# Performance work log

Measured on AMD Instinct MI355X. Metric: run time of the kernel, lower is better.

Reference implementation:

```python
import jax, jax.numpy as jnp
import numpy as np

B, T, C, H = 8, 2048, 1024, 64  # batch, seq_len, num_embed, size_head


def setup_inputs() -> dict:
    key = jax.random.key(0)
    kx, kq, kk, kv = jax.random.split(key, 4)
    return {
        "x": jax.random.normal(kx, (B, T, C), dtype=jnp.float32),
        "Wq": jax.random.normal(kq, (C, H), dtype=jnp.float32) * 0.02,
        "Wk": jax.random.normal(kk, (C, H), dtype=jnp.float32) * 0.02,
        "Wv": jax.random.normal(kv, (C, H), dtype=jnp.float32) * 0.02,
    }


def reference(x, Wq, Wk, Wv):
    # x: [B, T, C]; single-head causal self-attention.
    # NOTE: original scales by num_channels = x.shape[-1] (= C), not head dim.
    num_channels = x.shape[-1]
    q = jnp.einsum("btc,ch->bth", x, Wq)
    k = jnp.einsum("btc,ch->bth", x, Wk)
    v = jnp.einsum("btc,ch->bth", x, Wv)
    w = jnp.einsum("bqh,bkh->bqk", q, k) * (num_channels ** -0.5)  # [B,T,T]
    causal = jnp.tril(jnp.ones((x.shape[1], x.shape[1]), dtype=bool))
    w = jnp.where(causal, w, -jnp.inf)
    w = jax.nn.softmax(w, axis=-1)
    # dropout is identity in eval/reference mode
    out = jnp.einsum("bqk,bkh->bqh", w, v)  # [B,T,H]
    return out
```

## Files before the change

kernel.cpp:

```cpp
#include <hip/hip_runtime.h>
#include <hip/hip_bf16.h>
#include <stdint.h>

#define Bn 8
#define Tn 2048
#define Cn 1024
#define Hn 64

typedef __attribute__((ext_vector_type(8))) short bf16x8;
typedef __attribute__((ext_vector_type(4))) short bf16x4;
typedef __attribute__((ext_vector_type(4))) float f32x4;

#if defined(__HIP_DEVICE_COMPILE__) && !__has_builtin(__builtin_amdgcn_mfma_f32_16x16x16bf16_1k)
#error "mfma_f32_16x16x16bf16_1k required on gfx950"
#endif
#define MFMA16(a, b, c) __builtin_amdgcn_mfma_f32_16x16x16bf16_1k(a, b, c, 0, 0, 0)
#define MFMA32(a, b, c) __builtin_amdgcn_mfma_f32_16x16x32_bf16(a, b, c, 0, 0, 0)

__device__ __forceinline__ unsigned short f2bf(float f) {
  union { float f; unsigned int u; } v; v.f = f;
  unsigned int u = v.u;
  u = u + 0x7fffu + ((u >> 16) & 1u);
  return (unsigned short)(u >> 16);
}

__device__ __forceinline__ void gload16(const void* g, void* l) {
  __builtin_amdgcn_global_load_lds(
      (const __attribute__((address_space(1))) unsigned int*)g,
      (__attribute__((address_space(3))) unsigned int*)l, 16, 0, 0);
}

__global__ __launch_bounds__(256) void k_prep(const float* __restrict__ Wq,
                                              const float* __restrict__ Wk,
                                              const float* __restrict__ Wv,
                                              unsigned short* __restrict__ Wt) {
  const int m = blockIdx.x >> 6;
  const int h = blockIdx.x & 63;
  const float* W = (m == 0) ? Wq : (m == 1) ? Wk : Wv;
  const int tid = threadIdx.x;
  unsigned short* dst = Wt + ((size_t)(m * 64 + h)) * 1024;
#pragma unroll
  for (int j = 0; j < 4; ++j) {
    int c = j * 256 + tid;
    dst[c] = f2bf(W[(size_t)c * 64 + h]);
  }
}

__global__ __launch_bounds__(256, 1) void k_qkv(const float* __restrict__ x,
                                                const unsigned short* __restrict__ Wt,
                                                unsigned short* __restrict__ Q,
                                                unsigned short* __restrict__ K,
                                                unsigned short* __restrict__ Vt) {
  __shared__ __align__(16) char smem[81920];

  const int tid = threadIdx.x;
  const int lane = tid & 63;
  const int wid = __builtin_amdgcn_readfirstlane(tid >> 6);
  const int l15 = lane & 15, g = lane >> 4;
  const int r0 = blockIdx.x * 64;

  f32x4 acc[12];
#pragma unroll
  for (int j = 0; j < 12; ++j)
#pragma unroll
    for (int r = 0; r < 4; ++r) acc[j][r] = 0.f;

  auto stage = [&](int buf, int kt) {
    char* base = smem + buf * 40960;
    const int k0 = kt * 64;
#pragma unroll
    for (int j = 0; j < 4; ++j) {
      const int c = wid * 4 + j;
      const int row = c * 4 + (lane >> 4);
      const int lg = (lane & 15) ^ (row & 7);
      gload16(x + (size_t)(r0 + row) * 1024 + k0 + lg * 4,
              base + c * 1024);
    }
#pragma unroll
    for (int j = 0; j < 6; ++j) {
      const int c = j * 4 + wid;
      const int row = c * 8 + (lane >> 3);
      const int lg = (lane & 7) ^ (row & 7);
      gload16(Wt + (size_t)row * 1024 + k0 + lg * 8,
              base + 16384 + c * 1024);
    }
  };

  stage(0, 0);
  const int myrow = wid * 16 + l15;
  const int rs = myrow & 7;
  for (int kt = 0; kt < 16; ++kt) {
    const int cur = kt & 1;
    __syncthreads();
    if (kt < 15) stage(cur ^ 1, kt + 1);
    const char* base = smem + cur * 40960;
    const float* xf = (const float*)base;
    const unsigned short* wf = (const unsigned short*)(base + 16384);
#pragma unroll
    for (int kf = 0; kf < 2; ++kf) {
      f32x4 x0 = *(const f32x4*)&xf[myrow * 64 + (((kf * 8 + 2 * g) ^ rs) * 4)];
      f32x4 x1 = *(const f32x4*)&xf[myrow * 64 + (((kf * 8 + 2 * g + 1) ^ rs) * 4)];
      bf16x8 a;
      a[0] = (short)f2bf(x0[0]); a[1] = (short)f2bf(x0[1]);
      a[2] = (short)f2bf(x0[2]); a[3] = (short)f2bf(x0[3]);
      a[4] = (short)f2bf(x1[0]); a[5] = (short)f2bf(x1[1]);
      a[6] = (short)f2bf(x1[2]); a[7] = (short)f2bf(x1[3]);
#pragma unroll
      for (int nf = 0; nf < 12; ++nf) {
        const int row = nf * 16 + l15;
        bf16x8 b = *(const bf16x8*)&wf[row * 64 + (((kf * 4 + g) ^ (row & 7)) * 8)];
        acc[nf] = MFMA32(a, b, acc[nf]);
      }
    }
  }

  unsigned short (*os)[200] = (unsigned short (*)[200])smem;
#pragma unroll
  for (int nf = 0; nf < 12; ++nf)
#pragma unroll
    for (int r = 0; r < 4; ++r)
      os[wid * 16 + 4 * g + r][nf * 16 + l15] = f2bf(acc[nf][r]);
  __syncthreads();

  const int b = r0 >> 11;
  const int t0 = r0 & 2047;
#pragma unroll
  for (int j = 0; j < 2; ++j) {
    int u = j * 256 + tid;
    int row = u >> 3, ch = u & 7;
    *(uint4*)(Q + (size_t)(r0 + row) * 64 + ch * 8) = *(const uint4*)&os[row][ch * 8];
    *(uint4*)(K + (size_t)(r0 + row) * 64 + ch * 8) = *(const uint4*)&os[row][64 + ch * 8];
  }
#pragma unroll
  for (int j = 0; j < 2; ++j) {
    int u = j * 256 + tid;
    int h = u >> 3, tc = (u & 7) * 8;
    unsigned short tmp[8];
#pragma unroll
    for (int r = 0; r < 8; ++r) tmp[r] = os[tc + r][128 + h];
    *(uint4*)(Vt + ((size_t)b * 64 + h) * 2048 + t0 + tc) = *(const uint4*)tmp;
  }
}

__global__ __launch_bounds__(256, 3) void k_attn_coop(const unsigned short* __restrict__ Q,
                                                      const unsigned short* __restrict__ K,
                                                      const unsigned short* __restrict__ Vt,
                                                      float* __restrict__ out,
                                                      float* __restrict__ po,
                                                      float* __restrict__ pml) {
  __shared__ __align__(16) unsigned short lds[2][8192];

  const int tid = threadIdx.x;
  const int lane = tid & 63;
  const int l15 = lane & 15, g = lane >> 4;
  const int wid = __builtin_amdgcn_readfirstlane(tid >> 6);

  const int raw = blockIdx.x;
  const int bi = (raw & 7) * 144 + (raw >> 3);
  const int b = bi / 144;
  const int id = bi - b * 144;
  int gq = 0;
#pragma unroll
  for (int t = 1; t < 8; ++t)
    if (id >= 2 * t * (t + 1)) gq = t;
  const int rem = id - 2 * gq * (gq + 1);
  const int ql = rem / (gq + 1);
  const int s = rem - ql * (gq + 1);
  const int qt = 4 * gq + ql;
  const int qblk = qt * 64;
  const int klo = 256 * s;
  const int khi = min(klo + 256, qblk + 64);
  const int nt = (khi - klo + 63) >> 6;
  const int q0w = qblk + wid * 16;

  const unsigned short* Qb = Q + (size_t)b * Tn * Hn;
  const unsigned short* Kb = K + (size_t)b * Tn * Hn;
  const unsigned short* Vb = Vt + (size_t)b * Hn * Tn;

  bf16x8 bq0 = *(const bf16x8*)(Qb + (size_t)(q0w + l15) * 64 + g * 8);
  bf16x8 bq1 = *(const bf16x8*)(Qb + (size_t)(q0w + l15) * 64 + 32 + g * 8);

  f32x4 o[4];
#pragma unroll
  for (int hf = 0; hf < 4; ++hf)
#pragma unroll
    for (int r = 0; r < 4; ++r) o[hf][r] = 0.f;
  float m = -1e30f, lsum = 0.f;
  const float sc = 0.03125f * 1.44269504088896f;

  auto stage = [&](int buf, int k0) {
    unsigned short* tb = &lds[buf][0];
#pragma unroll
    for (int j = 0; j < 4; ++j) {
      const int p = wid * 256 + j * 64 + lane;
      const unsigned short* src;
      if (wid < 2) {
        const int row = p >> 3, c = p & 7;
        src = Kb + (size_t)(k0 + row) * 64 + ((c ^ (row & 7)) * 8);
      } else {
        const int q = p - 512;
        const int h = q >> 3, c = q & 7;
        src = Vb + (size_t)h * Tn + k0 + ((c ^ (h & 7)) * 8);
      }
      gload16(src, tb + wid * 2048 + j * 512);
    }
  };

  stage(0, klo);
  __syncthreads();

  for (int t = 0; t < nt; ++t) {
    const int cur = t & 1;
    const int k0 = klo + t * 64;
    if (t + 1 < nt) stage(cur ^ 1, klo + (t + 1) * 64);

    const unsigned short* kt = &lds[cur][0];
    const unsigned short* vt = &lds[cur][4096];

    f32x4 sacc[4];
#pragma unroll
    for (int kc = 0; kc < 4; ++kc) {
      const int row = kc * 16 + l15;
      const int sw = row & 7;
      bf16x8 ka = *(const bf16x8*)&kt[row * 64 + ((g ^ sw) * 8)];
      bf16x8 kb2 = *(const bf16x8*)&kt[row * 64 + (((4 + g) ^ sw) * 8)];
#pragma unroll
      for (int r = 0; r < 4; ++r) sacc[kc][r] = 0.f;
      sacc[kc] = MFMA32(ka, bq0, sacc[kc]);
      sacc[kc] = MFMA32(kb2, bq1, sacc[kc]);
    }
    float sv[4][4];
    if (k0 + 63 > q0w) {
      const int q = q0w + l15;
#pragma unroll
      for (int kc = 0; kc < 4; ++kc)
#pragma unroll
        for (int r = 0; r < 4; ++r) {
          int key = k0 + kc * 16 + 4 * g + r;
          sv[kc][r] = (key <= q) ? sacc[kc][r] * sc : -1e30f;
        }
    } else {
#pragma unroll
      for (int kc = 0; kc < 4; ++kc)
#pragma unroll
        for (int r = 0; r < 4; ++r) sv[kc][r] = sacc[kc][r] * sc;
    }
    float pm = sv[0][0];
#pragma unroll
    for (int kc = 0; kc < 4; ++kc)
#pragma unroll
      for (int r = 0; r < 4; ++r) pm = fmaxf(pm, sv[kc][r]);
    if (__any(pm > m + 8.f)) {
      pm = fmaxf(pm, __shfl_xor(pm, 16));
      pm = fmaxf(pm, __shfl_xor(pm, 32));
      float mn = fmaxf(m, pm);
      float alpha = exp2f(m - mn);
      lsum *= alpha;
      float an[4];
#pragma unroll
      for (int r = 0; r < 4; ++r) an[r] = __shfl(alpha, 4 * g + r);
#pragma unroll
      for (int hf = 0; hf < 4; ++hf)
#pragma unroll
        for (int r = 0; r < 4; ++r) o[hf][r] *= an[r];
      m = mn;
    }
    float ts = 0.f;
#pragma unroll
    for (int kc = 0; kc < 4; ++kc)
#pragma unroll
      for (int r = 0; r < 4; ++r) { sv[kc][r] = exp2f(sv[kc][r] - m); ts += sv[kc][r]; }
    ts += __shfl_xor(ts, 16);
    ts += __shfl_xor(ts, 32);
    lsum += ts;
    bf16x4 pa[4];
#pragma unroll
    for (int kc = 0; kc < 4; ++kc) {
      pa[kc][0] = (short)f2bf(sv[kc][0]); pa[kc][1] = (short)f2bf(sv[kc][1]);
      pa[kc][2] = (short)f2bf(sv[kc][2]); pa[kc][3] = (short)f2bf(sv[kc][3]);
    }
    bf16x4 vf[4][4];
#pragma unroll
    for (int hf = 0; hf < 4; ++hf) {
      const int h = hf * 16 + l15, hs = h & 7;
#pragma unroll
      for (int kc = 0; kc < 4; ++kc) {
        const int gran = (kc * 2 + (g >> 1)) ^ hs;
        vf[hf][kc] = *(const bf16x4*)&vt[h * 64 + gran * 8 + (g & 1) * 4];
      }
    }
#pragma unroll
    for (int hf = 0; hf < 4; ++hf)
#pragma unroll
      for (int kc = 0; kc < 4; ++kc)
        o[hf] = MFMA16(pa[kc], vf[hf][kc], o[hf]);

    __syncthreads();
  }

  if (qt >= 4) {
    const int slot = b * 140 + id - 4;
    float* pob = po + (size_t)slot * 4096;
#pragma unroll
    for (int hf = 0; hf < 4; ++hf)
#pragma unroll
      for (int r = 0; r < 4; ++r)
        pob[(16 * wid + 4 * g + r) * 64 + hf * 16 + l15] = o[hf][r];
    if (lane < 16) {
      pml[(size_t)slot * 128 + 16 * wid + l15] = m;
      pml[(size_t)slot * 128 + 64 + 16 * wid + l15] = lsum;
    }
  } else {
    const float il = 1.f / lsum;
    float iln[4];
#pragma unroll
    for (int r = 0; r < 4; ++r) iln[r] = __shfl(il, 4 * g + r);
    float* ob = out + ((size_t)b * Tn + q0w) * 64;
#pragma unroll
    for (int hf = 0; hf < 4; ++hf)
#pragma unroll
      for (int r = 0; r < 4; ++r)
        ob[(size_t)(4 * g + r) * 64 + hf * 16 + l15] = o[hf][r] * iln[r];
  }
}

__global__ __launch_bounds__(256) void k_comb(const float* __restrict__ po,
                                              const float* __restrict__ pml,
                                              float* __restrict__ out) {
  const int qt = 4 + blockIdx.x;
  const int b = blockIdx.y;
  const int gq = qt >> 2, ql = qt & 3;
  const int nseg = gq + 1;
  const int base = b * 140 + 2 * gq * (gq + 1) + ql * (gq + 1) - 4;
  const int r = threadIdx.x >> 2;
  const int cg = threadIdx.x & 3;

  float mv[8], lv[8], M = -1e30f;
#pragma unroll
  for (int s = 0; s < 8; ++s)
    if (s < nseg) {
      mv[s] = pml[(size_t)(base + s) * 128 + r];
      lv[s] = pml[(size_t)(base + s) * 128 + 64 + r];
      M = fmaxf(M, mv[s]);
    }
  float w[8], L = 0.f;
#pragma unroll
  for (int s = 0; s < 8; ++s)
    if (s < nseg) { w[s] = exp2f(mv[s] - M); L += w[s] * lv[s]; }

  float acc[16];
#pragma unroll
  for (int c = 0; c < 16; ++c) acc[c] = 0.f;
#pragma unroll
  for (int s = 0; s < 8; ++s)
    if (s < nseg) {
      const float* pb = po + (size_t)(base + s) * 4096 + r * 64 + cg * 16;
#pragma unroll
      for (int j = 0; j < 4; ++j) {
        float4 v = *(const float4*)(pb + 4 * j);
        acc[4 * j + 0] += w[s] * v.x; acc[4 * j + 1] += w[s] * v.y;
        acc[4 * j + 2] += w[s] * v.z; acc[4 * j + 3] += w[s] * v.w;
      }
    }
  const float invL = 1.f / L;
  float* ob = out + ((size_t)b * Tn + qt * 64 + r) * 64 + cg * 16;
#pragma unroll
  for (int j = 0; j < 4; ++j) {
    float4 v;
    v.x = acc[4 * j + 0] * invL; v.y = acc[4 * j + 1] * invL;
    v.z = acc[4 * j + 2] * invL; v.w = acc[4 * j + 3] * invL;
    *(float4*)(ob + 4 * j) = v;
  }
}

__global__ __launch_bounds__(256, 2) void k_attn_wave(const unsigned short* __restrict__ Q,
                                                      const unsigned short* __restrict__ K,
                                                      const unsigned short* __restrict__ Vt,
                                                      float* __restrict__ out) {
  const int tid = threadIdx.x;
  const int lane = tid & 63;
  const int l15 = lane & 15, g = lane >> 4;
  const int wid = tid >> 6;
  const int task = blockIdx.x * 4 + wid;
  const int b = task >> 7, qt = task & 127;
  const int q0 = qt * 16;
  const int nt = (q0 + 16 + 63) >> 6;

  const unsigned short* Qb = Q + (size_t)b * Tn * Hn;
  const unsigned short* Kb = K + (size_t)b * Tn * Hn;
  const unsigned short* Vb = Vt + (size_t)b * Hn * Tn;

  bf16x8 bq0 = *(const bf16x8*)(Qb + (size_t)(q0 + l15) * 64 + g * 8);
  bf16x8 bq1 = *(const bf16x8*)(Qb + (size_t)(q0 + l15) * 64 + 32 + g * 8);

  f32x4 o[4];
#pragma unroll
  for (int hf = 0; hf < 4; ++hf)
#pragma unroll
    for (int r = 0; r < 4; ++r) o[hf][r] = 0.f;
  float m = -1e30f, lsum = 0.f;
  const float sc = 0.03125f * 1.44269504088896f;

  for (int t = 0; t < nt; ++t) {
    const int k0 = t * 64;
    bf16x4 vf[4][4];
#pragma unroll
    for (int hf = 0; hf < 4; ++hf) {
      const unsigned short* vrow = Vb + (size_t)(hf * 16 + l15) * Tn + k0 + 4 * g;
#pragma unroll
      for (int kc = 0; kc < 4; ++kc) vf[hf][kc] = *(const bf16x4*)(vrow + kc * 16);
    }
    f32x4 sacc[4];
#pragma unroll
    for (int kc = 0; kc < 4; ++kc) {
      const unsigned short* kp = Kb + (size_t)(k0 + kc * 16 + l15) * 64 + g * 8;
      bf16x8 ka = *(const bf16x8*)kp;
      bf16x8 kb2 = *(const bf16x8*)(kp + 32);
#pragma unroll
      for (int r = 0; r < 4; ++r) sacc[kc][r] = 0.f;
      sacc[kc] = MFMA32(ka, bq0, sacc[kc]);
      sacc[kc] = MFMA32(kb2, bq1, sacc[kc]);
    }
    float sv[4][4];
    if (k0 + 63 > q0) {
      const int q = q0 + l15;
#pragma unroll
      for (int kc = 0; kc < 4; ++kc)
#pragma unroll
        for (int r = 0; r < 4; ++r) {
          int key = k0 + kc * 16 + 4 * g + r;
          sv[kc][r] = (key <= q) ? sacc[kc][r] * sc : -1e30f;
        }
    } else {
#pragma unroll
      for (int kc = 0; kc < 4; ++kc)
#pragma unroll
        for (int r = 0; r < 4; ++r) sv[kc][r] = sacc[kc][r] * sc;
    }
    float pm = sv[0][0];
#pragma unroll
    for (int kc = 0; kc < 4; ++kc)
#pragma unroll
      for (int r = 0; r < 4; ++r) pm = fmaxf(pm, sv[kc][r]);
    if (__any(pm > m + 8.f)) {
      pm = fmaxf(pm, __shfl_xor(pm, 16));
      pm = fmaxf(pm, __shfl_xor(pm, 32));
      float mn = fmaxf(m, pm);
      float alpha = exp2f(m - mn);
      lsum *= alpha;
      float an[4];
#pragma unroll
      for (int r = 0; r < 4; ++r) an[r] = __shfl(alpha, 4 * g + r);
#pragma unroll
      for (int hf = 0; hf < 4; ++hf)
#pragma unroll
        for (int r = 0; r < 4; ++r) o[hf][r] *= an[r];
      m = mn;
    }
    float ts = 0.f;
#pragma unroll
    for (int kc = 0; kc < 4; ++kc)
#pragma unroll
      for (int r = 0; r < 4; ++r) { sv[kc][r] = exp2f(sv[kc][r] - m); ts += sv[kc][r]; }
    ts += __shfl_xor(ts, 16);
    ts += __shfl_xor(ts, 32);
    lsum += ts;
    bf16x4 pa[4];
#pragma unroll
    for (int kc = 0; kc < 4; ++kc) {
      pa[kc][0] = (short)f2bf(sv[kc][0]); pa[kc][1] = (short)f2bf(sv[kc][1]);
      pa[kc][2] = (short)f2bf(sv[kc][2]); pa[kc][3] = (short)f2bf(sv[kc][3]);
    }
#pragma unroll
    for (int hf = 0; hf < 4; ++hf)
#pragma unroll
      for (int kc = 0; kc < 4; ++kc)
        o[hf] = MFMA16(pa[kc], vf[hf][kc], o[hf]);
  }
  const float il = 1.f / lsum;
  float iln[4];
#pragma unroll
  for (int r = 0; r < 4; ++r) iln[r] = __shfl(il, 4 * g + r);
  float* ob = out + ((size_t)b * Tn + q0) * 64;
#pragma unroll
  for (int hf = 0; hf < 4; ++hf)
#pragma unroll
    for (int r = 0; r < 4; ++r)
      ob[(size_t)(4 * g + r) * 64 + hf * 16 + l15] = o[hf][r] * iln[r];
}

extern "C" void kernel_launch(void* const* d_in, const int* in_sizes, int n_in,
                              void* d_out, int out_size, void* d_ws, size_t ws_size,
                              hipStream_t stream) {
  const float* x  = (const float*)d_in[0];
  const float* Wq = (const float*)d_in[1];
  const float* Wk = (const float*)d_in[2];
  const float* Wv = (const float*)d_in[3];
  float* out = (float*)d_out;

  unsigned short* Wt = (unsigned short*)d_ws;
  unsigned short* Qs = Wt + 3 * 64 * 1024;
  unsigned short* Ks = Qs + (size_t)Bn * Tn * Hn;
  unsigned short* Vt = Ks + (size_t)Bn * Tn * Hn;
  const size_t bf_bytes = (3 * 64 * 1024 + 3 * (size_t)Bn * Tn * Hn) * 2;
  float* po = (float*)((char*)d_ws + bf_bytes);

  const size_t nslots = (size_t)Bn * 140;
  float* pml = po + nslots * 4096;
  const size_t need = bf_bytes + nslots * (4096 + 128) * sizeof(float);

  hipLaunchKernelGGL(k_prep, dim3(192), dim3(256), 0, stream, Wq, Wk, Wv, Wt);
  hipLaunchKernelGGL(k_qkv, dim3(256), dim3(256), 0, stream, x, Wt, Qs, Ks, Vt);
  if (ws_size >= need) {
    hipLaunchKernelGGL(k_attn_coop, dim3(1152), dim3(256), 0, stream, Qs, Ks, Vt, out, po, pml);
    hipLaunchKernelGGL(k_comb, dim3(28, 8), dim3(256), 0, stream, po, pml, out);
  } else {
    hipLaunchKernelGGL(k_attn_wave, dim3(256), dim3(256), 0, stream, Qs, Ks, Vt, out);
  }
}
```

Before: 54.26 us.

## Split QKV projection across 16 waves per block with 4x4 wave grid

The QKV projection kernel moves from 4 waves to 16 waves per block, laid out as a 4x4 grid over rows and output columns, so each wave holds 3 accumulator tiles instead of 12. Staging loads and the epilogue stores are spread over all 1024 threads, and the barrier moves to the end of each k-step. This is meant to raise latency hiding and memory-level parallelism in a kernel that launches only 256 blocks. In exchange, each wave now converts the same x fragment to bf16 redundantly, and the larger block adds barrier cost.

```diff
diff --git a/kernel.cpp b/kernel.cpp
--- a/kernel.cpp
+++ b/kernel.cpp
@@ -46,52 +46,50 @@
   }
 }
 
-__global__ __launch_bounds__(256, 1) void k_qkv(const float* __restrict__ x,
-                                                const unsigned short* __restrict__ Wt,
-                                                unsigned short* __restrict__ Q,
-                                                unsigned short* __restrict__ K,
-                                                unsigned short* __restrict__ Vt) {
+__global__ __launch_bounds__(1024, 4) void k_qkv(const float* __restrict__ x,
+                                                 const unsigned short* __restrict__ Wt,
+                                                 unsigned short* __restrict__ Q,
+                                                 unsigned short* __restrict__ K,
+                                                 unsigned short* __restrict__ Vt) {
   __shared__ __align__(16) char smem[81920];
 
   const int tid = threadIdx.x;
   const int lane = tid & 63;
   const int wid = __builtin_amdgcn_readfirstlane(tid >> 6);
+  const int wm = wid >> 2, wn = wid & 3;
   const int l15 = lane & 15, g = lane >> 4;
   const int r0 = blockIdx.x * 64;
 
-  f32x4 acc[12];
-#pragma unroll
-  for (int j = 0; j < 12; ++j)
+  f32x4 acc[3];
+#pragma unroll
+  for (int j = 0; j < 3; ++j)
 #pragma unroll
     for (int r = 0; r < 4; ++r) acc[j][r] = 0.f;
 
   auto stage = [&](int buf, int kt) {
     char* base = smem + buf * 40960;
     const int k0 = kt * 64;
-#pragma unroll
-    for (int j = 0; j < 4; ++j) {
-      const int c = wid * 4 + j;
-      const int row = c * 4 + (lane >> 4);
-      const int lg = (lane & 15) ^ (row & 7);
-      gload16(x + (size_t)(r0 + row) * 1024 + k0 + lg * 4,
-              base + c * 1024);
-    }
-#pragma unroll
-    for (int j = 0; j < 6; ++j) {
-      const int c = j * 4 + wid;
-      const int row = c * 8 + (lane >> 3);
-      const int lg = (lane & 7) ^ (row & 7);
-      gload16(Wt + (size_t)row * 1024 + k0 + lg * 8,
-              base + 16384 + c * 1024);
+    for (int c = wid; c < 40; c += 16) {
+      if (c < 16) {
+        const int row = c * 4 + (lane >> 4);
+        const int lg = (lane & 15) ^ (row & 7);
+        gload16(x + (size_t)(r0 + row) * 1024 + k0 + lg * 4, base + c * 1024);
+      } else {
+        const int cw = c - 16;
+        const int row = cw * 8 + (lane >> 3);
+        const int lg = (lane & 7) ^ (row & 7);
+        gload16(Wt + (size_t)row * 1024 + k0 + lg * 8, base + 16384 + cw * 1024);
+      }
     }
   };
 
   stage(0, 0);
-  const int myrow = wid * 16 + l15;
+  __syncthreads();
+
+  const int myrow = wm * 16 + l15;
   const int rs = myrow & 7;
   for (int kt = 0; kt < 16; ++kt) {
     const int cur = kt & 1;
-    __syncthreads();
     if (kt < 15) stage(cur ^ 1, kt + 1);
     const char* base = smem + cur * 40960;
     const float* xf = (const float*)base;
@@ -106,39 +104,39 @@
       a[4] = (short)f2bf(x1[0]); a[5] = (short)f2bf(x1[1]);
       a[6] = (short)f2bf(x1[2]); a[7] = (short)f2bf(x1[3]);
 #pragma unroll
-      for (int nf = 0; nf < 12; ++nf) {
-        const int row = nf * 16 + l15;
+      for (int nf = 0; nf < 3; ++nf) {
+        const int row = wn * 48 + nf * 16 + l15;
         bf16x8 b = *(const bf16x8*)&wf[row * 64 + (((kf * 4 + g) ^ (row & 7)) * 8)];
         acc[nf] = MFMA32(a, b, acc[nf]);
       }
     }
+    __syncthreads();
   }
 
   unsigned short (*os)[200] = (unsigned short (*)[200])smem;
 #pragma unroll
-  for (int nf = 0; nf < 12; ++nf)
+  for (int nf = 0; nf < 3; ++nf)
 #pragma unroll
     for (int r = 0; r < 4; ++r)
-      os[wid * 16 + 4 * g + r][nf * 16 + l15] = f2bf(acc[nf][r]);
+      os[wm * 16 + 4 * g + r][wn * 48 + nf * 16 + l15] = f2bf(acc[nf][r]);
   __syncthreads();
 
   const int b = r0 >> 11;
   const int t0 = r0 & 2047;
-#pragma unroll
-  for (int j = 0; j < 2; ++j) {
-    int u = j * 256 + tid;
+  {
+    int u = tid & 511;
     int row = u >> 3, ch = u & 7;
-    *(uint4*)(Q + (size_t)(r0 + row) * 64 + ch * 8) = *(const uint4*)&os[row][ch * 8];
-    *(uint4*)(K + (size_t)(r0 + row) * 64 + ch * 8) = *(const uint4*)&os[row][64 + ch * 8];
-  }
-#pragma unroll
-  for (int j = 0; j < 2; ++j) {
-    int u = j * 256 + tid;
-    int h = u >> 3, tc = (u & 7) * 8;
-    unsigned short tmp[8];
-#pragma unroll
-    for (int r = 0; r < 8; ++r) tmp[r] = os[tc + r][128 + h];
-    *(uint4*)(Vt + ((size_t)b * 64 + h) * 2048 + t0 + tc) = *(const uint4*)tmp;
+    if (tid < 512)
+      *(uint4*)(Q + (size_t)(r0 + row) * 64 + ch * 8) = *(const uint4*)&os[row][ch * 8];
+    else
+      *(uint4*)(K + (size_t)(r0 + row) * 64 + ch * 8) = *(const uint4*)&os[row][64 + ch * 8];
+  }
+  {
+    int h = tid >> 4, tq = (tid & 15) * 4;
+    unsigned short tmp[4];
+#pragma unroll
+    for (int r = 0; r < 4; ++r) tmp[r] = os[tq + r][128 + h];
+    *(ushort4*)(Vt + ((size_t)b * 64 + h) * 2048 + t0 + tq) = *(const ushort4*)tmp;
   }
 }
 
@@ -510,7 +508,7 @@
   const size_t need = bf_bytes + nslots * (4096 + 128) * sizeof(float);
 
   hipLaunchKernelGGL(k_prep, dim3(192), dim3(256), 0, stream, Wq, Wk, Wv, Wt);
-  hipLaunchKernelGGL(k_qkv, dim3(256), dim3(256), 0, stream, x, Wt, Qs, Ks, Vt);
+  hipLaunchKernelGGL(k_qkv, dim3(256), dim3(1024), 0, stream, x, Wt, Qs, Ks, Vt);
   if (ws_size >= need) {
     hipLaunchKernelGGL(k_attn_coop, dim3(1152), dim3(256), 0, stream, Qs, Ks, Vt, out, po, pml);
     hipLaunchKernelGGL(k_comb, dim3(28, 8), dim3(256), 0, stream, po, pml, out);
```

Result: no change. 53.80 us (-0.8%).
